# Kernel tuning notes

Measured on AMD Instinct MI355X. Metric: run time of the kernel, lower is better.

The kernel has to match this reference:

```python
import jax, jax.numpy as jnp
import numpy as np

DIM = 1024
HEADS = 16
DIM_HEAD = 64
B, N = 2, 2048
EPS_NORM = 1e-12  # F.normalize clamp


def setup_inputs() -> dict:
    key = jax.random.key(0)
    k1, k2, k3 = jax.random.split(key, 3)
    x = jax.random.normal(k1, (B, N, DIM), dtype=jnp.float32)
    gamma = jnp.ones((DIM,), dtype=jnp.float32)
    w_qkv = jax.random.normal(k2, (DIM, 3 * HEADS * DIM_HEAD), dtype=jnp.float32) * (DIM ** -0.5)
    w_out = jax.random.normal(k3, (HEADS * DIM_HEAD, DIM), dtype=jnp.float32) * (DIM ** -0.5)
    return {"x": x, "gamma": gamma, "w_qkv": w_qkv, "w_out": w_out}


def reference(x, gamma, w_qkv, w_out):
    b, n, dim = x.shape
    h, dh = HEADS, DIM_HEAD
    # RMSNorm: F.normalize(x, dim=-1) * sqrt(dim) * gamma
    norm = jnp.maximum(jnp.linalg.norm(x, axis=-1, keepdims=True), EPS_NORM)
    normed = x / norm * (dim ** 0.5) * gamma
    # qkv projection (no bias)
    qkv = normed @ w_qkv  # [b, n, 3*h*dh]
    qkv = qkv.reshape(b, n, 3, h, dh)
    q = qkv[:, :, 0].transpose(0, 2, 1, 3)  # [b, h, n, dh]
    k = qkv[:, :, 1].transpose(0, 2, 1, 3)
    v = qkv[:, :, 2].transpose(0, 2, 1, 3)
    q = q * (dh ** -0.5)
    # attention scores
    sim = jnp.einsum('bhid,bhjd->bhij', q, k)
    mask_value = -jnp.finfo(sim.dtype).max
    # causal mask: triu with offset j - i + 1 (here i == j == n -> offset 1)
    causal_mask = jnp.triu(jnp.ones((n, n), dtype=bool), 1)
    sim = jnp.where(causal_mask, mask_value, sim)
    attn = jax.nn.softmax(sim, axis=-1)
    out = jnp.einsum('bhij,bhjd->bhid', attn, v)
    out = out.transpose(0, 2, 1, 3).reshape(b, n, h * dh)
    return out @ w_out
```

## Files before the change

kernel.cpp:

```cpp
#include <hip/hip_runtime.h>
#include <hip/hip_bf16.h>

typedef unsigned short u16;
using bf16x8 = __attribute__((ext_vector_type(8))) short;
using f32x4  = __attribute__((ext_vector_type(4))) float;
using f32x16 = __attribute__((ext_vector_type(16))) float;
using u32x4  = __attribute__((ext_vector_type(4))) unsigned int;

constexpr int B_ = 2, N_ = 2048, DIM_ = 1024, H_ = 16, DH_ = 64;
constexpr int M_ = B_ * N_;
constexpr int NCQ = 3 * H_ * DH_;

__device__ inline u16 f2bf(float f) {
  union { float f; unsigned u; } v{f};
  unsigned r = v.u + 0x7FFF + ((v.u >> 16) & 1);
  return (u16)(r >> 16);
}

__device__ __forceinline__ void st_pair(u16* p0, u16* p1, float a, float b) {
  unsigned w;
  asm("v_cvt_pk_bf16_f32 %0, %1, %2" : "=v"(w) : "v"(a), "v"(b));
  *p0 = (u16)w;
  *p1 = (u16)(w >> 16);
}

__device__ __forceinline__ void gload16(const u16* g, u16* l) {
  __builtin_amdgcn_global_load_lds(
      (const __attribute__((address_space(1))) unsigned int*)g,
      (__attribute__((address_space(3))) unsigned int*)l, 16, 0, 0);
}

__global__ void __launch_bounds__(256) rmsnorm_kernel(const float* __restrict__ x,
                                                      const float* __restrict__ gamma,
                                                      u16* __restrict__ out) {
  int row = blockIdx.x;
  int t = threadIdx.x;
  const float4 v = reinterpret_cast<const float4*>(x + (size_t)row * DIM_)[t];
  float ss = v.x * v.x + v.y * v.y + v.z * v.z + v.w * v.w;
#pragma unroll
  for (int o = 32; o; o >>= 1) ss += __shfl_down(ss, o, 64);
  __shared__ float partial[4];
  int wid = t >> 6, lane = t & 63;
  if (lane == 0) partial[wid] = ss;
  __syncthreads();
  float tot = partial[0] + partial[1] + partial[2] + partial[3];
  float norm = fmaxf(sqrtf(tot), 1e-12f);
  float scale = 32.0f / norm;
  const float4 g = reinterpret_cast<const float4*>(gamma)[t];
  ushort4 o4;
  o4.x = f2bf(v.x * scale * g.x);
  o4.y = f2bf(v.y * scale * g.y);
  o4.z = f2bf(v.z * scale * g.z);
  o4.w = f2bf(v.w * scale * g.w);
  reinterpret_cast<ushort4*>(out + (size_t)row * DIM_)[t] = o4;
}

__global__ void __launch_bounds__(256) transpose_w_kernel(const float* __restrict__ W,
                                                          u16* __restrict__ WT,
                                                          int K, int Nc) {
  __shared__ float tile[32][33];
  int bc = blockIdx.x * 32;
  int bk = blockIdx.y * 32;
  int tx = threadIdx.x & 31, ty = threadIdx.x >> 5;
#pragma unroll
  for (int r = ty; r < 32; r += 8)
    tile[r][tx] = W[(size_t)(bk + r) * Nc + bc + tx];
  __syncthreads();
#pragma unroll
  for (int r = ty; r < 32; r += 8)
    WT[(size_t)(bc + r) * K + bk + tx] = f2bf(tile[tx][r]);
}

template <int MODE>
__global__ void __launch_bounds__(256) gemm2_kernel(const u16* __restrict__ A,
                                                    const u16* __restrict__ BT,
                                                    void* __restrict__ Cv,
                                                    u16* __restrict__ q_s,
                                                    u16* __restrict__ k_s,
                                                    u16* __restrict__ vt,
                                                    int M, int Nc, int K) {
  __shared__ alignas(16) u16 smem[16384];
  int tid = threadIdx.x;
  int lane = tid & 63, wid = tid >> 6;
  int lr = lane & 15, g = lane >> 4;
  int am0 = (wid >> 1) * 64;
  int bn0 = (wid & 1) * 64;
  int rbase_a = blockIdx.y * 128;
  int rbase_b = blockIdx.x * 128;

  int lineo = tid >> 3;
  int p = tid & 7;
  f32x4 acc[4][4] = {};

#define GSTAGE(base_, src_, rb_, k0_) do {                                           \
    _Pragma("unroll")                                                                \
    for (int c = 0; c < 2; c++) {                                                    \
      int line = c * 32 + lineo;                                                     \
      int sp = p ^ (line & 7);                                                       \
      int row = 2 * line + (sp >> 2);                                                \
      int j = sp & 3;                                                                \
      gload16(src_ + (size_t)(rb_ + row) * K + (k0_) + j * 8,                        \
              (base_) + c * 2048 + wid * 512);                                       \
    }                                                                                \
  } while (0)

#define STAGE(ib_, k0_) do {                                                         \
    GSTAGE(smem + (ib_) * 4096, A, rbase_a, k0_);                                    \
    GSTAGE(smem + 8192 + (ib_) * 4096, BT, rbase_b, k0_);                            \
  } while (0)

  int steps = K >> 5;
  STAGE(0, 0);
  for (int t = 0; t < steps; ++t) {
    int ibuf = t & 1;
    if (t + 1 < steps) {
      STAGE(ibuf ^ 1, (t + 1) * 32);
      asm volatile("s_waitcnt vmcnt(4)" ::: "memory");
    } else {
      asm volatile("s_waitcnt vmcnt(0)" ::: "memory");
    }
    __builtin_amdgcn_s_barrier();
    __builtin_amdgcn_sched_barrier(0);

    const char* ab = (const char*)(smem + ibuf * 4096);
    const char* bb = (const char*)(smem + 8192 + ibuf * 4096);
    bf16x8 a[4], b[4];
#pragma unroll
    for (int mi = 0; mi < 4; mi++) {
      int row = am0 + mi * 16 + lr;
      int byte = (row >> 1) * 128 + ((((row & 1) << 2) + g) ^ ((row >> 1) & 7)) * 16;
      a[mi] = *reinterpret_cast<const bf16x8*>(ab + byte);
    }
#pragma unroll
    for (int ni = 0; ni < 4; ni++) {
      int row = bn0 + ni * 16 + lr;
      int byte = (row >> 1) * 128 + ((((row & 1) << 2) + g) ^ ((row >> 1) & 7)) * 16;
      b[ni] = *reinterpret_cast<const bf16x8*>(bb + byte);
    }
#pragma unroll
    for (int mi = 0; mi < 4; mi++)
#pragma unroll
      for (int ni = 0; ni < 4; ni++)
        acc[mi][ni] = __builtin_amdgcn_mfma_f32_16x16x32_bf16(a[mi], b[ni], acc[mi][ni], 0, 0, 0);

    __builtin_amdgcn_sched_barrier(0);
    __builtin_amdgcn_s_barrier();
  }

  int orow = g * 4;
  if (MODE == 1) {
#pragma unroll
    for (int mi = 0; mi < 4; mi++)
#pragma unroll
      for (int ni = 0; ni < 4; ni++)
#pragma unroll
        for (int r = 0; r < 4; r++) {
          int row = rbase_a + am0 + 16 * mi + orow + r;
          int col = rbase_b + bn0 + 16 * ni + lr;
          ((float*)Cv)[(size_t)row * Nc + col] = acc[mi][ni][r];
        }
  } else {
    int colbase = rbase_b + bn0;
    int region = colbase >> 10;
    int head = (colbase >> 6) & 15;
    const float QS = 0.125f * 1.4426950408889634f;
    if (region < 2) {
#pragma unroll
      for (int mi = 0; mi < 4; mi++)
#pragma unroll
        for (int ni = 0; ni < 4; ni++)
#pragma unroll
          for (int r = 0; r < 4; r += 2) {
            int row = rbase_a + am0 + 16 * mi + orow + r;
            int n = row & 2047, bb_ = row >> 11;
            float v0 = acc[mi][ni][r], v1 = acc[mi][ni][r + 1];
            size_t d0 = ((size_t)(bb_ * 16 + head) * 2048 + n) * 64 + 16 * ni + lr;
            if (region == 0)
              st_pair(q_s + d0, q_s + d0 + 64, v0 * QS, v1 * QS);
            else
              st_pair(k_s + d0, k_s + d0 + 64, v0, v1);
          }
    } else {
      u16* tlds = smem + wid * 4096;
      int n_base = (rbase_a + am0) & 2047;
      int bq = (rbase_a + am0) >> 11;
#pragma unroll
      for (int mi = 0; mi < 4; mi++)
#pragma unroll
        for (int ni = 0; ni < 4; ni++) {
          int n_loc = mi * 16 + orow;
          int dh_loc = ni * 16 + lr;
          unsigned w0, w1;
          asm("v_cvt_pk_bf16_f32 %0, %1, %2"
              : "=v"(w0) : "v"(acc[mi][ni][0]), "v"(acc[mi][ni][1]));
          asm("v_cvt_pk_bf16_f32 %0, %1, %2"
              : "=v"(w1) : "v"(acc[mi][ni][2]), "v"(acc[mi][ni][3]));
          int byte = dh_loc * 128 + ((n_loc * 2) ^ ((dh_loc & 7) << 4));
          uint2 val; val.x = w0; val.y = w1;
          *reinterpret_cast<uint2*>((char*)tlds + byte) = val;
        }
#pragma unroll
      for (int it = 0; it < 8; it++) {
        int dh_loc = it * 8 + (lane >> 3);
        int n8 = (lane & 7) * 8;
        int byte = dh_loc * 128 + ((n8 * 2) ^ ((dh_loc & 7) << 4));
        bf16x8 v = *reinterpret_cast<const bf16x8*>((const char*)tlds + byte);
        size_t dst = ((size_t)(bq * 16 + head) * 64 + dh_loc) * 2048 + n_base + n8;
        *reinterpret_cast<bf16x8*>(vt + dst) = v;
      }
    }
  }
#undef STAGE
#undef GSTAGE
}

__global__ void __launch_bounds__(128) attn7_kernel(const u16* __restrict__ q_s,
                                                    const u16* __restrict__ k_s,
                                                    const u16* __restrict__ vt,
                                                    u16* __restrict__ ao) {
  __shared__ alignas(16) u16 smem[16384];
  int tid = threadIdx.x;
  int lane = tid & 63, myhalf = tid >> 6;
  int q31 = lane & 31, hi = lane >> 5;
  int blk = blockIdx.x;
  int bh = blk & 31;
  int jq = 63 - (blk >> 5);
  int b = bh >> 4, h = bh & 15;
  const u16* qp = q_s + (size_t)bh * N_ * DH_;
  const u16* kp = k_s + (size_t)bh * N_ * DH_;
  const u16* vp = vt + (size_t)bh * DH_ * N_;
  int q0w = jq * 32;
  int qi = q0w + q31;
  int steps = (jq >> 1) + 1;

  bf16x8 qf[4];
#pragma unroll
  for (int c = 0; c < 4; c++)
    qf[c] = *reinterpret_cast<const bf16x8*>(qp + (size_t)(q0w + q31) * 64 + c * 16 + hi * 8);

  f32x16 o0 = {}, o1 = {};
  float lsum = 0.f;

  int srow = lane >> 3;
  int scol = (lane & 7) ^ srow;

#define STAGE(ib_, kv0_) do {                                                                \
    _Pragma("unroll")                                                                        \
    for (int cc = 0; cc < 4; cc++) {                                                         \
      int c = myhalf * 4 + cc;                                                               \
      gload16(kp + (size_t)((kv0_) + c * 8 + srow) * 64 + scol * 8,                          \
              smem + (ib_) * 4096 + c * 512);                                                \
      gload16(vp + (size_t)(c * 8 + srow) * N_ + (kv0_) + scol * 8,                          \
              smem + 8192 + (ib_) * 4096 + c * 512);                                         \
    }                                                                                        \
  } while (0)

  STAGE(0, 0);

  for (int t = 0; t < steps; ++t) {
    int ibuf = t & 1;
    if (t + 1 < steps) {
      STAGE(ibuf ^ 1, (t + 1) * 64);
      asm volatile("s_waitcnt vmcnt(8)" ::: "memory");
    } else {
      asm volatile("s_waitcnt vmcnt(0)" ::: "memory");
    }
    __builtin_amdgcn_s_barrier();
    __builtin_amdgcn_sched_barrier(0);

    const u16* kb = smem + ibuf * 4096;
    const u16* vb = smem + 8192 + ibuf * 4096;
    int kv = t * 64 + myhalf * 32;
    if (kv <= q0w + 31) {
      f32x16 st = {};
      int krow = myhalf * 32 + q31;
      int ksw = (krow & 7) << 4;
      __builtin_amdgcn_s_setprio(1);
#pragma unroll
      for (int c = 0; c < 4; c++) {
        bf16x8 kf = *reinterpret_cast<const bf16x8*>(
            (const char*)kb + krow * 128 + (((c * 2 + hi) * 16) ^ ksw));
        st = __builtin_amdgcn_mfma_f32_32x32x16_bf16(kf, qf[c], st, 0, 0, 0);
      }
      __builtin_amdgcn_s_setprio(0);
      float p[16];
      bool diag = (kv + 31 > q0w);
      if (diag) {
#pragma unroll
        for (int r = 0; r < 16; r++) {
          int key = kv + (r & 3) + 8 * (r >> 2) + 4 * hi;
          float e = __builtin_amdgcn_exp2f(st[r]);
          p[r] = (key > qi) ? 0.f : e;
        }
      } else {
#pragma unroll
        for (int r = 0; r < 16; r++) p[r] = __builtin_amdgcn_exp2f(st[r]);
      }
#pragma unroll
      for (int r = 0; r < 16; r++) lsum += p[r];
      unsigned cw0[4], cw1[4];
#pragma unroll
      for (int jj = 0; jj < 4; jj++) {
        asm("v_cvt_pk_bf16_f32 %0, %1, %2" : "=v"(cw0[jj]) : "v"(p[4 * jj]), "v"(p[4 * jj + 1]));
        asm("v_cvt_pk_bf16_f32 %0, %1, %2" : "=v"(cw1[jj]) : "v"(p[4 * jj + 2]), "v"(p[4 * jj + 3]));
      }
#pragma unroll
      for (int kc = 0; kc < 2; kc++) {
        unsigned c0a = cw0[2 * kc], c0b = cw0[2 * kc + 1];
        unsigned c1a = cw1[2 * kc], c1b = cw1[2 * kc + 1];
        unsigned sel0 = hi ? c0a : c0b;
        unsigned sel1 = hi ? c1a : c1b;
        unsigned r0 = (unsigned)__shfl_xor((int)sel0, 32, 64);
        unsigned r1 = (unsigned)__shfl_xor((int)sel1, 32, 64);
        u32x4 w;
        w[0] = hi ? r0 : c0a;
        w[1] = hi ? r1 : c1a;
        w[2] = hi ? c0b : r0;
        w[3] = hi ? c1b : r1;
        bf16x8 pa = __builtin_bit_cast(bf16x8, w);
        int slot = (myhalf * 4 + kc * 2 + hi) * 16;
        int vsw = (q31 & 7) << 4;
        bf16x8 vf0 = *reinterpret_cast<const bf16x8*>(
            (const char*)vb + q31 * 128 + (slot ^ vsw));
        bf16x8 vf1 = *reinterpret_cast<const bf16x8*>(
            (const char*)vb + (32 + q31) * 128 + (slot ^ vsw));
        __builtin_amdgcn_s_setprio(1);
        o0 = __builtin_amdgcn_mfma_f32_32x32x16_bf16(pa, vf0, o0, 0, 0, 0);
        o1 = __builtin_amdgcn_mfma_f32_32x32x16_bf16(pa, vf1, o1, 0, 0, 0);
        __builtin_amdgcn_s_setprio(0);
      }
    }
    __builtin_amdgcn_sched_barrier(0);
    __builtin_amdgcn_s_barrier();
  }

  __syncthreads();
  float lc = lsum + __shfl_xor(lsum, 32, 64);
  float* cb = (float*)smem;
  if (myhalf) {
#pragma unroll
    for (int r = 0; r < 16; r++) {
      cb[r * 64 + lane] = o0[r];
      cb[(16 + r) * 64 + lane] = o1[r];
    }
    cb[2048 + lane] = lc;
  }
  __syncthreads();
  if (!myhalf) {
#pragma unroll
    for (int r = 0; r < 16; r++) {
      o0[r] += cb[r * 64 + lane];
      o1[r] += cb[(16 + r) * 64 + lane];
    }
    float ltot = fmaxf(lc + cb[2048 + lane], 1e-30f);
    float linv = 1.0f / ltot;
#pragma unroll
    for (int r = 0; r < 16; r += 2) {
      int qrow0 = (r & 3) + 8 * (r >> 2) + 4 * hi;
      float li0 = __shfl(linv, qrow0, 64);
      float li1 = __shfl(linv, qrow0 + 1, 64);
      size_t base0 = (size_t)(b * N_ + q0w + qrow0) * 1024 + h * 64;
      st_pair(ao + base0 + q31, ao + base0 + 1024 + q31, o0[r] * li0, o0[r + 1] * li1);
      st_pair(ao + base0 + 32 + q31, ao + base0 + 1024 + 32 + q31, o1[r] * li0, o1[r + 1] * li1);
    }
  }
#undef STAGE
}

extern "C" void kernel_launch(void* const* d_in, const int* in_sizes, int n_in,
                              void* d_out, int out_size, void* d_ws, size_t ws_size,
                              hipStream_t stream) {
  const float* x = (const float*)d_in[0];
  const float* gamma = (const float*)d_in[1];
  const float* w_qkv = (const float*)d_in[2];
  const float* w_out = (const float*)d_in[3];
  float* out = (float*)d_out;

  char* p = (char*)d_ws;
  u16* normed = (u16*)p; p += (size_t)M_ * DIM_ * 2;
  u16* wt_qkv = (u16*)p; p += (size_t)NCQ * DIM_ * 2;
  u16* wt_out = (u16*)p; p += (size_t)DIM_ * DIM_ * 2;
  u16* k_s = (u16*)p;    p += (size_t)M_ * DIM_ * 2;
  u16* vt = (u16*)p;     p += (size_t)M_ * DIM_ * 2;
  u16* q_s = (u16*)p;    p += (size_t)M_ * DIM_ * 2;
  u16* ao = (u16*)p;     p += (size_t)M_ * DIM_ * 2;

  hipLaunchKernelGGL(rmsnorm_kernel, dim3(M_), dim3(256), 0, stream, x, gamma, normed);
  hipLaunchKernelGGL(transpose_w_kernel, dim3(NCQ / 32, DIM_ / 32), dim3(256), 0, stream,
                     w_qkv, wt_qkv, DIM_, NCQ);
  hipLaunchKernelGGL(transpose_w_kernel, dim3(DIM_ / 32, DIM_ / 32), dim3(256), 0, stream,
                     w_out, wt_out, DIM_, DIM_);
  hipLaunchKernelGGL(gemm2_kernel<2>, dim3(NCQ / 128, M_ / 128), dim3(256), 0, stream,
                     normed, wt_qkv, nullptr, q_s, k_s, vt, M_, NCQ, DIM_);
  hipLaunchKernelGGL(attn7_kernel, dim3(B_ * H_ * (N_ / 32)), dim3(128), 0, stream,
                     q_s, k_s, vt, ao);
  hipLaunchKernelGGL(gemm2_kernel<1>, dim3(DIM_ / 128, M_ / 128), dim3(256), 0, stream,
                     ao, wt_out, (void*)out, nullptr, nullptr, nullptr, M_, DIM_, DIM_);
}
```

Before: 116.5 us.

## Load K/V directly from global into registers, dropping LDS staging and barriers

The attention kernel no longer stages K and V tiles through double-buffered shared memory with block-wide barriers. Each wave now reads its K fragments and V fragments straight from global memory into registers, alternating between 32-key tiles and prefetching the next K tile into a second register set. This removes the LDS round trip and the per-step barriers, and cuts shared memory down to the small final reduction buffer so more blocks can fit per CU. In exchange, V reads are strided 16-byte loads from global or L2 with no coalescing through LDS, and only K is prefetched, so V load latency may be exposed.

```diff
diff --git a/kernel.cpp b/kernel.cpp
--- a/kernel.cpp
+++ b/kernel.cpp
@@ -214,11 +214,11 @@
 #undef GSTAGE
 }
 
-__global__ void __launch_bounds__(128) attn7_kernel(const u16* __restrict__ q_s,
+__global__ void __launch_bounds__(128) attn8_kernel(const u16* __restrict__ q_s,
                                                     const u16* __restrict__ k_s,
                                                     const u16* __restrict__ vt,
                                                     u16* __restrict__ ao) {
-  __shared__ alignas(16) u16 smem[16384];
+  __shared__ float cb[2112];
   int tid = threadIdx.x;
   int lane = tid & 63, myhalf = tid >> 6;
   int q31 = lane & 31, hi = lane >> 5;
@@ -231,7 +231,7 @@
   const u16* vp = vt + (size_t)bh * DH_ * N_;
   int q0w = jq * 32;
   int qi = q0w + q31;
-  int steps = (jq >> 1) + 1;
+  int ntiles = jq + 1;
 
   bf16x8 qf[4];
 #pragma unroll
@@ -241,102 +241,88 @@
   f32x16 o0 = {}, o1 = {};
   float lsum = 0.f;
 
-  int srow = lane >> 3;
-  int scol = (lane & 7) ^ srow;
-
-#define STAGE(ib_, kv0_) do {                                                                \
-    _Pragma("unroll")                                                                        \
-    for (int cc = 0; cc < 4; cc++) {                                                         \
-      int c = myhalf * 4 + cc;                                                               \
-      gload16(kp + (size_t)((kv0_) + c * 8 + srow) * 64 + scol * 8,                          \
-              smem + (ib_) * 4096 + c * 512);                                                \
-      gload16(vp + (size_t)(c * 8 + srow) * N_ + (kv0_) + scol * 8,                          \
-              smem + 8192 + (ib_) * 4096 + c * 512);                                         \
-    }                                                                                        \
-  } while (0)
-
-  STAGE(0, 0);
-
-  for (int t = 0; t < steps; ++t) {
-    int ibuf = t & 1;
-    if (t + 1 < steps) {
-      STAGE(ibuf ^ 1, (t + 1) * 64);
-      asm volatile("s_waitcnt vmcnt(8)" ::: "memory");
+  const u16* kbase = kp + (size_t)q31 * 64 + hi * 8;
+  const u16* vb0 = vp + (size_t)q31 * 2048 + hi * 8;
+  const u16* vb1 = vb0 + (size_t)32 * 2048;
+
+  auto loadK = [&](bf16x8 (&kf)[4], int kv) {
+#pragma unroll
+    for (int c = 0; c < 4; c++)
+      kf[c] = *reinterpret_cast<const bf16x8*>(kbase + (size_t)kv * 64 + c * 16);
+  };
+
+  auto compute = [&](const bf16x8 (&kf)[4], int t_) {
+    int kv = t_ * 32;
+    bf16x8 vf[2][2];
+#pragma unroll
+    for (int kc = 0; kc < 2; kc++) {
+      vf[kc][0] = *reinterpret_cast<const bf16x8*>(vb0 + kv + kc * 16);
+      vf[kc][1] = *reinterpret_cast<const bf16x8*>(vb1 + kv + kc * 16);
+    }
+    f32x16 st = {};
+    __builtin_amdgcn_s_setprio(1);
+#pragma unroll
+    for (int c = 0; c < 4; c++)
+      st = __builtin_amdgcn_mfma_f32_32x32x16_bf16(kf[c], qf[c], st, 0, 0, 0);
+    __builtin_amdgcn_s_setprio(0);
+    float p[16];
+    if (t_ == jq) {
+#pragma unroll
+      for (int r = 0; r < 16; r++) {
+        int key = kv + (r & 3) + 8 * (r >> 2) + 4 * hi;
+        float e = __builtin_amdgcn_exp2f(st[r]);
+        p[r] = (key > qi) ? 0.f : e;
+      }
     } else {
-      asm volatile("s_waitcnt vmcnt(0)" ::: "memory");
-    }
-    __builtin_amdgcn_s_barrier();
-    __builtin_amdgcn_sched_barrier(0);
-
-    const u16* kb = smem + ibuf * 4096;
-    const u16* vb = smem + 8192 + ibuf * 4096;
-    int kv = t * 64 + myhalf * 32;
-    if (kv <= q0w + 31) {
-      f32x16 st = {};
-      int krow = myhalf * 32 + q31;
-      int ksw = (krow & 7) << 4;
+#pragma unroll
+      for (int r = 0; r < 16; r++) p[r] = __builtin_amdgcn_exp2f(st[r]);
+    }
+#pragma unroll
+    for (int r = 0; r < 16; r++) lsum += p[r];
+    unsigned cw0[4], cw1[4];
+#pragma unroll
+    for (int jj = 0; jj < 4; jj++) {
+      asm("v_cvt_pk_bf16_f32 %0, %1, %2" : "=v"(cw0[jj]) : "v"(p[4 * jj]), "v"(p[4 * jj + 1]));
+      asm("v_cvt_pk_bf16_f32 %0, %1, %2" : "=v"(cw1[jj]) : "v"(p[4 * jj + 2]), "v"(p[4 * jj + 3]));
+    }
+#pragma unroll
+    for (int kc = 0; kc < 2; kc++) {
+      unsigned c0a = cw0[2 * kc], c0b = cw0[2 * kc + 1];
+      unsigned c1a = cw1[2 * kc], c1b = cw1[2 * kc + 1];
+      unsigned sel0 = hi ? c0a : c0b;
+      unsigned sel1 = hi ? c1a : c1b;
+      unsigned r0 = (unsigned)__shfl_xor((int)sel0, 32, 64);
+      unsigned r1 = (unsigned)__shfl_xor((int)sel1, 32, 64);
+      u32x4 w;
+      w[0] = hi ? r0 : c0a;
+      w[1] = hi ? r1 : c1a;
+      w[2] = hi ? c0b : r0;
+      w[3] = hi ? c1b : r1;
+      bf16x8 pa = __builtin_bit_cast(bf16x8, w);
       __builtin_amdgcn_s_setprio(1);
-#pragma unroll
-      for (int c = 0; c < 4; c++) {
-        bf16x8 kf = *reinterpret_cast<const bf16x8*>(
-            (const char*)kb + krow * 128 + (((c * 2 + hi) * 16) ^ ksw));
-        st = __builtin_amdgcn_mfma_f32_32x32x16_bf16(kf, qf[c], st, 0, 0, 0);
-      }
+      o0 = __builtin_amdgcn_mfma_f32_32x32x16_bf16(pa, vf[kc][0], o0, 0, 0, 0);
+      o1 = __builtin_amdgcn_mfma_f32_32x32x16_bf16(pa, vf[kc][1], o1, 0, 0, 0);
       __builtin_amdgcn_s_setprio(0);
-      float p[16];
-      bool diag = (kv + 31 > q0w);
-      if (diag) {
-#pragma unroll
-        for (int r = 0; r < 16; r++) {
-          int key = kv + (r & 3) + 8 * (r >> 2) + 4 * hi;
-          float e = __builtin_amdgcn_exp2f(st[r]);
-          p[r] = (key > qi) ? 0.f : e;
-        }
-      } else {
-#pragma unroll
-        for (int r = 0; r < 16; r++) p[r] = __builtin_amdgcn_exp2f(st[r]);
-      }
-#pragma unroll
-      for (int r = 0; r < 16; r++) lsum += p[r];
-      unsigned cw0[4], cw1[4];
-#pragma unroll
-      for (int jj = 0; jj < 4; jj++) {
-        asm("v_cvt_pk_bf16_f32 %0, %1, %2" : "=v"(cw0[jj]) : "v"(p[4 * jj]), "v"(p[4 * jj + 1]));
-        asm("v_cvt_pk_bf16_f32 %0, %1, %2" : "=v"(cw1[jj]) : "v"(p[4 * jj + 2]), "v"(p[4 * jj + 3]));
-      }
-#pragma unroll
-      for (int kc = 0; kc < 2; kc++) {
-        unsigned c0a = cw0[2 * kc], c0b = cw0[2 * kc + 1];
-        unsigned c1a = cw1[2 * kc], c1b = cw1[2 * kc + 1];
-        unsigned sel0 = hi ? c0a : c0b;
-        unsigned sel1 = hi ? c1a : c1b;
-        unsigned r0 = (unsigned)__shfl_xor((int)sel0, 32, 64);
-        unsigned r1 = (unsigned)__shfl_xor((int)sel1, 32, 64);
-        u32x4 w;
-        w[0] = hi ? r0 : c0a;
-        w[1] = hi ? r1 : c1a;
-        w[2] = hi ? c0b : r0;
-        w[3] = hi ? c1b : r1;
-        bf16x8 pa = __builtin_bit_cast(bf16x8, w);
-        int slot = (myhalf * 4 + kc * 2 + hi) * 16;
-        int vsw = (q31 & 7) << 4;
-        bf16x8 vf0 = *reinterpret_cast<const bf16x8*>(
-            (const char*)vb + q31 * 128 + (slot ^ vsw));
-        bf16x8 vf1 = *reinterpret_cast<const bf16x8*>(
-            (const char*)vb + (32 + q31) * 128 + (slot ^ vsw));
-        __builtin_amdgcn_s_setprio(1);
-        o0 = __builtin_amdgcn_mfma_f32_32x32x16_bf16(pa, vf0, o0, 0, 0, 0);
-        o1 = __builtin_amdgcn_mfma_f32_32x32x16_bf16(pa, vf1, o1, 0, 0, 0);
-        __builtin_amdgcn_s_setprio(0);
-      }
-    }
-    __builtin_amdgcn_sched_barrier(0);
-    __builtin_amdgcn_s_barrier();
-  }
-
-  __syncthreads();
+    }
+  };
+
+  int t = myhalf;
+  if (t < ntiles) {
+    bf16x8 kA[4], kB[4];
+    loadK(kA, t * 32);
+    while (true) {
+      if (t + 2 < ntiles) loadK(kB, (t + 2) * 32);
+      compute(kA, t);
+      t += 2;
+      if (t >= ntiles) break;
+      if (t + 2 < ntiles) loadK(kA, (t + 2) * 32);
+      compute(kB, t);
+      t += 2;
+      if (t >= ntiles) break;
+    }
+  }
+
   float lc = lsum + __shfl_xor(lsum, 32, 64);
-  float* cb = (float*)smem;
   if (myhalf) {
 #pragma unroll
     for (int r = 0; r < 16; r++) {
@@ -364,7 +350,6 @@
       st_pair(ao + base0 + 32 + q31, ao + base0 + 1024 + 32 + q31, o1[r] * li0, o1[r + 1] * li1);
     }
   }
-#undef STAGE
 }
 
 extern "C" void kernel_launch(void* const* d_in, const int* in_sizes, int n_in,
@@ -392,7 +377,7 @@
                      w_out, wt_out, DIM_, DIM_);
   hipLaunchKernelGGL(gemm2_kernel<2>, dim3(NCQ / 128, M_ / 128), dim3(256), 0, stream,
                      normed, wt_qkv, nullptr, q_s, k_s, vt, M_, NCQ, DIM_);
-  hipLaunchKernelGGL(attn7_kernel, dim3(B_ * H_ * (N_ / 32)), dim3(128), 0, stream,
+  hipLaunchKernelGGL(attn8_kernel, dim3(B_ * H_ * (N_ / 32)), dim3(128), 0, stream,
                      q_s, k_s, vt, ao);
   hipLaunchKernelGGL(gemm2_kernel<1>, dim3(DIM_ / 128, M_ / 128), dim3(256), 0, stream,
                      ao, wt_out, (void*)out, nullptr, nullptr, nullptr, M_, DIM_, DIM_);
```

Measured after the change: 134.1 us. +15.1%, slower.
